# Performance work log

Measured on AMD Instinct MI355X. Metric: run time of the kernel, lower is better.

The kernel has to match this reference:

```python
import jax, jax.numpy as jnp
import numpy as np

EMBED_DIM = 1024
HEAD_DIM = 64


def setup_inputs() -> dict:
    key = jax.random.key(0)
    ks = jax.random.split(key, 7)
    B, S = 4, 2048
    s = 1.0 / np.sqrt(EMBED_DIM)
    h = jax.random.normal(ks[0], (B, S, EMBED_DIM), dtype=jnp.float32)
    Wq = jax.random.normal(ks[1], (EMBED_DIM, HEAD_DIM), dtype=jnp.float32) * s
    bq = jax.random.normal(ks[2], (HEAD_DIM,), dtype=jnp.float32) * 0.01
    Wk = jax.random.normal(ks[3], (EMBED_DIM, HEAD_DIM), dtype=jnp.float32) * s
    bk = jax.random.normal(ks[4], (HEAD_DIM,), dtype=jnp.float32) * 0.01
    Wv = jax.random.normal(ks[5], (EMBED_DIM, HEAD_DIM), dtype=jnp.float32) * s
    bv = jax.random.normal(ks[6], (HEAD_DIM,), dtype=jnp.float32) * 0.01
    return {"h": h, "Wq": Wq, "bq": bq, "Wk": Wk, "bk": bk, "Wv": Wv, "bv": bv}


def reference(h, Wq, bq, Wk, bk, Wv, bv):
    # Linear projections: h [B,S,E] -> q,k [B,S,D]
    q = jnp.einsum("bse,ed->bsd", h, Wq) + bq
    k = jnp.einsum("bse,ed->bsd", h, Wk) + bk
    v = jnp.einsum("bse,ed->bsd", h, Wv) + bv  # computed but UNUSED (faithful to source)
    del v
    scale = 1.0 / jnp.sqrt(jnp.asarray(HEAD_DIM, dtype=q.dtype))
    # scores [B, Sq, Sk]
    scores = jnp.einsum("bqd,bkd->bqk", q, k) * scale
    # NOTE: source uses softmax over dim=1 (query axis), not the key axis
    weights = jax.nn.softmax(scores, axis=1)
    # NOTE: source passes h (not v) as the value tensor
    out = jnp.einsum("bqk,bke->bqe", weights, h)  # [B, Sq, E]
    return out
```

## Files before the change

kernel.cpp:

```cpp
#include <hip/hip_runtime.h>
#include <hip/hip_bf16.h>
#include <math.h>

#define EMBED 1024
#define HDIM  64
#define BATCH 4
#define SEQ   2048

typedef __attribute__((ext_vector_type(8))) short short8;
typedef __attribute__((ext_vector_type(4))) float f32x4;
typedef unsigned int u32;
typedef unsigned short u16;

static __device__ __forceinline__ u16 f2bf(float f) {
    union { float f; u32 u; } v; v.f = f;
    u32 r = v.u + 0x7fffu + ((v.u >> 16) & 1u);
    return (u16)(r >> 16);
}

static __device__ __forceinline__ void gload_lds16(const u16* g, u16* l) {
    __builtin_amdgcn_global_load_lds(
        (const __attribute__((address_space(1))) u32*)g,
        (__attribute__((address_space(3))) u32*)l, 16, 0, 0);
}

__global__ __launch_bounds__(256) void wt_kernel(
    const float* __restrict__ Wq, const float* __restrict__ Wk,
    u16* __restrict__ WqT, u16* __restrict__ WkT, float* __restrict__ lsum)
{
    __shared__ float tile[64][65];
    const float* W = blockIdx.y ? Wk : Wq;
    u16* WT = blockIdx.y ? WkT : WqT;
    int e0 = blockIdx.x * 64;
    int t = threadIdx.x, c = t & 63, r4 = t >> 6;
    lsum[(blockIdx.y * 16 + blockIdx.x) * 256 + t] = 0.f;
    for (int r = r4; r < 64; r += 4)
        tile[r][c] = W[(size_t)(e0 + r) * HDIM + c];
    __syncthreads();
    for (int d = r4; d < 64; d += 4)
        WT[(size_t)d * EMBED + e0 + c] = f2bf(tile[c][d]);
}

__global__ __launch_bounds__(256) void proj_kernel(
    const float* __restrict__ h, const u16* __restrict__ WqT, const u16* __restrict__ WkT,
    const float* __restrict__ bq, const float* __restrict__ bk,
    u16* __restrict__ Qbf, u16* __restrict__ Kbf)
{
    __shared__ u16 hs[2][16][136];
    int b = blockIdx.x >> 7, s0 = (blockIdx.x & 127) * 16;
    int t = threadIdx.x, lane = t & 63, w = t >> 6;
    int l15 = lane & 15, quad = lane >> 4;
    int pj = w >> 1, nh = (w & 1) * 32;
    const float* hb = h + ((size_t)b * SEQ + s0) * EMBED;
    const u16* Wp = pj ? WkT : WqT;
    int r = t >> 4, c4 = (t & 15) * 4;

    f32x4 preA0 = *(const f32x4*)(hb + (size_t)r * EMBED + c4);
    f32x4 preA1 = *(const f32x4*)(hb + (size_t)r * EMBED + 64 + c4);
    f32x4 preB0 = *(const f32x4*)(hb + (size_t)r * EMBED + 128 + c4);
    f32x4 preB1 = *(const f32x4*)(hb + (size_t)r * EMBED + 192 + c4);
    f32x4 accA[2], accB[2];
    accA[0] = accA[1] = accB[0] = accB[1] = (f32x4){0.f, 0.f, 0.f, 0.f};

    const u16* Wrow0 = Wp + (size_t)(nh + l15) * EMBED;
    const u16* Wrow1 = Wp + (size_t)(nh + 16 + l15) * EMBED;

    short8 cw[8];
#pragma unroll
    for (int i = 0; i < 4; i++) {
        cw[i]     = *(const short8*)(Wrow0 + i * 32 + quad * 8);
        cw[4 + i] = *(const short8*)(Wrow1 + i * 32 + quad * 8);
    }

    for (int it = 0; it < 8; ++it) {
        int ec = it * 128, buf = it & 1;
        uint2 pk;
        pk.x = (u32)f2bf(preA0[0]) | ((u32)f2bf(preA0[1]) << 16);
        pk.y = (u32)f2bf(preA0[2]) | ((u32)f2bf(preA0[3]) << 16);
        *(uint2*)&hs[buf][r][c4] = pk;
        pk.x = (u32)f2bf(preA1[0]) | ((u32)f2bf(preA1[1]) << 16);
        pk.y = (u32)f2bf(preA1[2]) | ((u32)f2bf(preA1[3]) << 16);
        *(uint2*)&hs[buf][r][64 + c4] = pk;
        __syncthreads();

        preA0 = preB0; preA1 = preB1;
        if (it + 2 < 8) {
            preB0 = *(const f32x4*)(hb + (size_t)r * EMBED + ec + 256 + c4);
            preB1 = *(const f32x4*)(hb + (size_t)r * EMBED + ec + 320 + c4);
        }
        short8 nw[8];
#pragma unroll
        for (int i = 0; i < 8; i++) nw[i] = cw[i];
        if (it + 1 < 8) {
#pragma unroll
            for (int i = 0; i < 4; i++) {
                nw[i]     = *(const short8*)(Wrow0 + ec + 128 + i * 32 + quad * 8);
                nw[4 + i] = *(const short8*)(Wrow1 + ec + 128 + i * 32 + quad * 8);
            }
        }

        short8 a0 = *(const short8*)&hs[buf][l15][quad * 8];
        short8 a1 = *(const short8*)&hs[buf][l15][32 + quad * 8];
        short8 a2 = *(const short8*)&hs[buf][l15][64 + quad * 8];
        short8 a3 = *(const short8*)&hs[buf][l15][96 + quad * 8];
        accA[0] = __builtin_amdgcn_mfma_f32_16x16x32_bf16(a0, cw[0], accA[0], 0, 0, 0);
        accA[1] = __builtin_amdgcn_mfma_f32_16x16x32_bf16(a0, cw[4], accA[1], 0, 0, 0);
        accB[0] = __builtin_amdgcn_mfma_f32_16x16x32_bf16(a1, cw[1], accB[0], 0, 0, 0);
        accB[1] = __builtin_amdgcn_mfma_f32_16x16x32_bf16(a1, cw[5], accB[1], 0, 0, 0);
        accA[0] = __builtin_amdgcn_mfma_f32_16x16x32_bf16(a2, cw[2], accA[0], 0, 0, 0);
        accA[1] = __builtin_amdgcn_mfma_f32_16x16x32_bf16(a2, cw[6], accA[1], 0, 0, 0);
        accB[0] = __builtin_amdgcn_mfma_f32_16x16x32_bf16(a3, cw[3], accB[0], 0, 0, 0);
        accB[1] = __builtin_amdgcn_mfma_f32_16x16x32_bf16(a3, cw[7], accB[1], 0, 0, 0);
#pragma unroll
        for (int i = 0; i < 8; i++) cw[i] = nw[i];
    }

    const float* bias = pj ? bk : bq;
    float scale = pj ? 1.0f : 0.125f;
    u16* outp = pj ? Kbf : Qbf;
    float bv0 = bias[nh + l15], bv1 = bias[nh + 16 + l15];
#pragma unroll
    for (int rr = 0; rr < 4; rr++) {
        size_t row = (size_t)b * SEQ + s0 + quad * 4 + rr;
        outp[row * HDIM + nh + l15]      = f2bf((accA[0][rr] + accB[0][rr] + bv0) * scale);
        outp[row * HDIM + nh + 16 + l15] = f2bf((accA[1][rr] + accB[1][rr] + bv1) * scale);
    }
}

__global__ __launch_bounds__(512) void sw_kernel(
    const u16* __restrict__ Qbf, const u16* __restrict__ Kbf,
    u16* __restrict__ Wmat, float* __restrict__ lsum)
{
    int b = blockIdx.z;
    int k0 = blockIdx.x * 64;
    int t = threadIdx.x, lane = t & 63, w = t >> 6;
    int l15 = lane & 15, quad = lane >> 4;
    const u16* Qb = Qbf + (size_t)b * SEQ * HDIM;
    const u16* Kb = Kbf + (size_t)b * SEQ * HDIM;
    u16* Wb = Wmat + (size_t)b * SEQ * SEQ;

    short8 kfr[4][2];
#pragma unroll
    for (int g = 0; g < 4; g++)
#pragma unroll
        for (int hh = 0; hh < 2; hh++)
            kfr[g][hh] = *(const short8*)(
                Kb + (size_t)(k0 + g * 16 + l15) * HDIM + hh * 32 + quad * 8);

    f32x4 lacc[4];
#pragma unroll
    for (int g = 0; g < 4; g++) lacc[g] = (f32x4){0.f, 0.f, 0.f, 0.f};

    int qs = (blockIdx.y * 8 + w) * 64;

#pragma unroll
    for (int half = 0; half < 2; ++half) {
        int q0 = qs + half * 32;
        short8 cf[2][2];
#pragma unroll
        for (int a = 0; a < 2; a++)
#pragma unroll
            for (int hh = 0; hh < 2; hh++)
                cf[a][hh] = *(const short8*)(
                    Qb + (size_t)(q0 + a * 16 + l15) * HDIM + hh * 32 + quad * 8);

        f32x4 acc[2][4];
#pragma unroll
        for (int a = 0; a < 2; a++)
#pragma unroll
            for (int g = 0; g < 4; g++) acc[a][g] = (f32x4){0.f, 0.f, 0.f, 0.f};
#pragma unroll
        for (int a = 0; a < 2; a++)
#pragma unroll
            for (int g = 0; g < 4; g++) {
                acc[a][g] = __builtin_amdgcn_mfma_f32_16x16x32_bf16(
                    kfr[g][0], cf[a][0], acc[a][g], 0, 0, 0);
                acc[a][g] = __builtin_amdgcn_mfma_f32_16x16x32_bf16(
                    kfr[g][1], cf[a][1], acc[a][g], 0, 0, 0);
            }
#pragma unroll
        for (int a = 0; a < 2; a++) {
            u16* wrow = Wb + (size_t)(q0 + a * 16 + l15) * SEQ + k0;
#pragma unroll
            for (int g = 0; g < 4; g++) {
                float e0 = __expf(acc[a][g][0]), e1 = __expf(acc[a][g][1]);
                float e2 = __expf(acc[a][g][2]), e3 = __expf(acc[a][g][3]);
                lacc[g][0] += e0; lacc[g][1] += e1;
                lacc[g][2] += e2; lacc[g][3] += e3;
                uint2 pk;
                pk.x = (u32)f2bf(e0) | ((u32)f2bf(e1) << 16);
                pk.y = (u32)f2bf(e2) | ((u32)f2bf(e3) << 16);
                *(uint2*)(wrow + g * 16 + quad * 4) = pk;
            }
        }
    }
#pragma unroll
    for (int m = 1; m <= 8; m <<= 1)
#pragma unroll
        for (int g = 0; g < 4; g++) {
            lacc[g][0] += __shfl_xor(lacc[g][0], m, 64);
            lacc[g][1] += __shfl_xor(lacc[g][1], m, 64);
            lacc[g][2] += __shfl_xor(lacc[g][2], m, 64);
            lacc[g][3] += __shfl_xor(lacc[g][3], m, 64);
        }
    if (l15 == 0) {
        float* lp = lsum + b * SEQ + k0 + quad * 4;
#pragma unroll
        for (int g = 0; g < 4; g++) {
            atomicAdd(lp + g * 16 + 0, lacc[g][0]);
            atomicAdd(lp + g * 16 + 1, lacc[g][1]);
            atomicAdd(lp + g * 16 + 2, lacc[g][2]);
            atomicAdd(lp + g * 16 + 3, lacc[g][3]);
        }
    }
}

__global__ __launch_bounds__(256) void tscale_kernel(
    const float* __restrict__ h, const float* __restrict__ lsum,
    u16* __restrict__ hT)
{
    __shared__ float tile[64][65];
    int b  = blockIdx.z;
    int s0 = blockIdx.x * 64, e0 = blockIdx.y * 64;
    int t = threadIdx.x;
    int r16 = t >> 4, c4 = (t & 15) * 4;
    const float* hb = h + (size_t)b * SEQ * EMBED;
#pragma unroll
    for (int rr = r16; rr < 64; rr += 16) {
        f32x4 v = *(const f32x4*)(hb + (size_t)(s0 + rr) * EMBED + e0 + c4);
        *(f32x4*)&tile[rr][c4] = v;
    }
    __syncthreads();
    f32x4 ls = *(const f32x4*)(lsum + b * SEQ + s0 + c4);
    f32x4 il4;
    il4[0] = __builtin_amdgcn_rcpf(ls[0]);
    il4[1] = __builtin_amdgcn_rcpf(ls[1]);
    il4[2] = __builtin_amdgcn_rcpf(ls[2]);
    il4[3] = __builtin_amdgcn_rcpf(ls[3]);
    u16* hTb = hT + (size_t)b * EMBED * SEQ;
#pragma unroll
    for (int er = r16; er < 64; er += 16) {
        u16 p0 = f2bf(tile[c4 + 0][er] * il4[0]);
        u16 p1 = f2bf(tile[c4 + 1][er] * il4[1]);
        u16 p2 = f2bf(tile[c4 + 2][er] * il4[2]);
        u16 p3 = f2bf(tile[c4 + 3][er] * il4[3]);
        uint2 pk;
        pk.x = (u32)p0 | ((u32)p1 << 16);
        pk.y = (u32)p2 | ((u32)p3 << 16);
        *(uint2*)(hTb + (size_t)(e0 + er) * SEQ + s0 + c4) = pk;
    }
}

__global__ __launch_bounds__(512, 2) void out_gemm_kernel(
    const u16* __restrict__ Wmat, const u16* __restrict__ hT, float* __restrict__ out)
{
    __shared__ __align__(16) char smem[3 * 49152];
    int b = blockIdx.z;
    int q0 = blockIdx.x * 256, e0 = blockIdx.y * 128;
    int t = threadIdx.x, lane = t & 63, w = t >> 6;
    int l15 = lane & 15, quad = lane >> 4;
    const u16* Wb  = Wmat + (size_t)b * SEQ * SEQ;
    const u16* hTb = hT + (size_t)b * EMBED * SEQ;
    int kf = w >> 2;
    int wm = (w >> 1) & 1, wn = w & 1;
    int wq = wm * 128, we = wn * 64;

    f32x4 acc[8][4];
#pragma unroll
    for (int i = 0; i < 8; i++)
#pragma unroll
        for (int j = 0; j < 4; j++) acc[i][j] = (f32x4){0.f, 0.f, 0.f, 0.f};

    int st_rl = lane >> 3;
    int st_pc = lane & 7;

    const u16* gA[4];
    const u16* gB[2];
#pragma unroll
    for (int ld = 0; ld < 4; ld++) {
        int row = w * 32 + ld * 8 + st_rl;
        int cg  = st_pc ^ (row & 7);
        gA[ld] = Wb + (size_t)(q0 + row) * SEQ + cg * 8;
    }
#pragma unroll
    for (int ld = 0; ld < 2; ld++) {
        int row = w * 16 + ld * 8 + st_rl;
        int cg  = st_pc ^ (row & 7);
        gB[ld] = hTb + (size_t)(e0 + row) * SEQ + cg * 8;
    }
    int dA[4], dB[2];
#pragma unroll
    for (int ld = 0; ld < 4; ld++) dA[ld] = (w * 32 + ld * 8) * 128 + lane * 16;
#pragma unroll
    for (int ld = 0; ld < 2; ld++) dB[ld] = 32768 + (w * 16 + ld * 8) * 128 + lane * 16;
    int offA[8], offB[4];
#pragma unroll
    for (int ii = 0; ii < 8; ii++) {
        int ra  = wq + ii * 16 + l15;
        int pca = (kf * 4 + quad) ^ (ra & 7);
        offA[ii] = ra * 128 + pca * 16;
    }
#pragma unroll
    for (int j = 0; j < 4; j++) {
        int rb  = we + j * 16 + l15;
        int pcb = (kf * 4 + quad) ^ (rb & 7);
        offB[j] = 32768 + rb * 128 + pcb * 16;
    }

#define STAGE_H1(si)                                                           \
    {                                                                          \
        gload_lds16(gA[0], (u16*)(smem + (si) * 49152 + dA[0]));               \
        gload_lds16(gA[1], (u16*)(smem + (si) * 49152 + dA[1]));               \
        gload_lds16(gB[0], (u16*)(smem + (si) * 49152 + dB[0]));               \
    }
#define STAGE_H2(si)                                                           \
    {                                                                          \
        gload_lds16(gA[2], (u16*)(smem + (si) * 49152 + dA[2]));               \
        gload_lds16(gA[3], (u16*)(smem + (si) * 49152 + dA[3]));               \
        gload_lds16(gB[1], (u16*)(smem + (si) * 49152 + dB[1]));               \
    }
#define ADV()                                                                  \
    {                                                                          \
        gA[0] += 64; gA[1] += 64; gA[2] += 64; gA[3] += 64;                    \
        gB[0] += 64; gB[1] += 64;                                              \
    }

#define MFMA16(i0)                                                             \
    {                                                                          \
        _Pragma("unroll")                                                      \
        for (int ii = 0; ii < 4; ii++)                                         \
            _Pragma("unroll")                                                  \
            for (int j = 0; j < 4; j++)                                        \
                acc[(i0) + ii][j] = __builtin_amdgcn_mfma_f32_16x16x32_bf16(   \
                    af[ii], bfr[j], acc[(i0) + ii][j], 0, 0, 0);               \
    }

#define TILE(si, si2, DO_STAGE, VMC)                                           \
    {                                                                          \
        const char* Sb = smem + (si) * 49152;                                  \
        short8 af[4], bfr[4];                                                  \
                                                                  \
        _Pragma("unroll")                                                      \
        for (int ii = 0; ii < 4; ii++)                                         \
            af[ii] = *(const short8*)(Sb + offA[ii]);                          \
        _Pragma("unroll")                                                      \
        for (int j = 0; j < 4; j++)                                            \
            bfr[j] = *(const short8*)(Sb + offB[j]);                           \
        if (DO_STAGE) STAGE_H1(si2)                                            \
        __builtin_amdgcn_s_barrier();                                          \
        asm volatile("s_waitcnt lgkmcnt(0)" ::: "memory");                     \
        __builtin_amdgcn_sched_barrier(0);                                     \
        __builtin_amdgcn_s_setprio(1);                                         \
        MFMA16(0)                                                              \
        __builtin_amdgcn_s_setprio(0);                                         \
        __builtin_amdgcn_s_barrier();                                          \
                                                                  \
        _Pragma("unroll")                                                      \
        for (int ii = 0; ii < 4; ii++)                                         \
            af[ii] = *(const short8*)(Sb + offA[4 + ii]);                      \
        if (DO_STAGE) { STAGE_H2(si2) ADV() }                                  \
        __builtin_amdgcn_s_barrier();                                          \
        asm volatile("s_waitcnt lgkmcnt(0)" ::: "memory");                     \
        __builtin_amdgcn_sched_barrier(0);                                     \
        __builtin_amdgcn_s_setprio(1);                                         \
        MFMA16(4)                                                              \
        __builtin_amdgcn_s_setprio(0);                                         \
        if ((VMC) == 6) { asm volatile("s_waitcnt vmcnt(6)" ::: "memory"); }   \
        else if ((VMC) == 0) { asm volatile("s_waitcnt vmcnt(0)" ::: "memory"); } \
        __builtin_amdgcn_s_barrier();                                          \
    }

    STAGE_H1(0) STAGE_H2(0) ADV()
    STAGE_H1(1) STAGE_H2(1) ADV()
    asm volatile("s_waitcnt vmcnt(6)" ::: "memory");
    __builtin_amdgcn_s_barrier();

    for (int g = 0; g < 10; ++g) {
        TILE(0, 2, true, 6)
        TILE(1, 0, true, 6)
        TILE(2, 1, true, 6)
    }
    TILE(0, 2, false, 0)
    TILE(1, 0, false, -1)
#undef TILE
#undef STAGE_H1
#undef STAGE_H2
#undef ADV
#undef MFMA16

    float* red = (float*)smem;
    if (w >= 4) {
        float* reg = red + (size_t)(w & 3) * 8192;
#pragma unroll
        for (int i = 0; i < 8; i++)
#pragma unroll
            for (int j = 0; j < 4; j++)
                *(f32x4*)(reg + ((i * 4 + j) * 64 + lane) * 4) = acc[i][j];
    }
    __syncthreads();
    if (w < 4) {
        float* reg = red + (size_t)w * 8192;
        float* outb = out + (size_t)b * SEQ * EMBED;
#pragma unroll
        for (int i = 0; i < 8; i++)
#pragma unroll
            for (int j = 0; j < 4; j++) {
                f32x4 o = *(const f32x4*)(reg + ((i * 4 + j) * 64 + lane) * 4);
                o += acc[i][j];
#pragma unroll
                for (int r = 0; r < 4; r++)
                    outb[(size_t)(q0 + wq + i * 16 + quad * 4 + r) * EMBED
                         + e0 + we + j * 16 + l15] = o[r];
            }
    }
}

extern "C" void kernel_launch(void* const* d_in, const int* in_sizes, int n_in,
                              void* d_out, int out_size, void* d_ws, size_t ws_size,
                              hipStream_t stream) {
    (void)in_sizes; (void)n_in; (void)out_size; (void)ws_size;
    const float* h  = (const float*)d_in[0];
    const float* Wq = (const float*)d_in[1];
    const float* bq = (const float*)d_in[2];
    const float* Wk = (const float*)d_in[3];
    const float* bk = (const float*)d_in[4];
    float* out = (float*)d_out;

    char* ws = (char*)d_ws;
    u16*   Qbf  = (u16*)(ws);
    u16*   Kbf  = (u16*)(ws + (1ull << 20));
    u16*   hT   = (u16*)(ws + (2ull << 20));
    float* lsum = (float*)(ws + (18ull << 20));
    u16*   WqT  = (u16*)(ws + (18ull << 20) + (128ull << 10));
    u16*   WkT  = (u16*)(ws + (18ull << 20) + (256ull << 10));
    u16*   Wmat = (u16*)(ws + (19ull << 20));

    hipLaunchKernelGGL(wt_kernel, dim3(16, 2), dim3(256), 0, stream,
                       Wq, Wk, WqT, WkT, lsum);
    hipLaunchKernelGGL(proj_kernel, dim3(512), dim3(256), 0, stream,
                       h, WqT, WkT, bq, bk, Qbf, Kbf);
    hipLaunchKernelGGL(sw_kernel, dim3(32, 4, 4), dim3(512), 0, stream,
                       Qbf, Kbf, Wmat, lsum);
    hipLaunchKernelGGL(tscale_kernel, dim3(32, 16, 4), dim3(256), 0, stream,
                       h, lsum, hT);
    hipLaunchKernelGGL(out_gemm_kernel, dim3(8, 8, 4), dim3(512), 0, stream,
                       Wmat, hT, out);
}
```

Before: 171.8 us.

## Recompute exp(QK^T) inside output GEMM instead of materializing weight matrix

Stops writing the bf16 exp(scores) matrix (B*S*S) to global memory. The column-sum pass becomes an LSE-only kernel, and the output GEMM recomputes exp(QK^T) per K tile in shared memory from Q registers and staged K. This removes a 32MB write and the matching read, at the cost of computing QK^T and exp twice and adding a barrier inside every tile. The GEMM tile changes to 128x256 with no split-K reduction, and the LDS layout changes to match.

```diff
diff --git a/kernel.cpp b/kernel.cpp
--- a/kernel.cpp
+++ b/kernel.cpp
@@ -127,9 +127,9 @@
     }
 }
 
-__global__ __launch_bounds__(512) void sw_kernel(
+__global__ __launch_bounds__(512) void lse_kernel(
     const u16* __restrict__ Qbf, const u16* __restrict__ Kbf,
-    u16* __restrict__ Wmat, float* __restrict__ lsum)
+    float* __restrict__ lsum)
 {
     int b = blockIdx.z;
     int k0 = blockIdx.x * 64;
@@ -137,7 +137,6 @@
     int l15 = lane & 15, quad = lane >> 4;
     const u16* Qb = Qbf + (size_t)b * SEQ * HDIM;
     const u16* Kb = Kbf + (size_t)b * SEQ * HDIM;
-    u16* Wb = Wmat + (size_t)b * SEQ * SEQ;
 
     short8 kfr[4][2];
 #pragma unroll
@@ -179,20 +178,14 @@
                     kfr[g][1], cf[a][1], acc[a][g], 0, 0, 0);
             }
 #pragma unroll
-        for (int a = 0; a < 2; a++) {
-            u16* wrow = Wb + (size_t)(q0 + a * 16 + l15) * SEQ + k0;
+        for (int a = 0; a < 2; a++)
 #pragma unroll
             for (int g = 0; g < 4; g++) {
-                float e0 = __expf(acc[a][g][0]), e1 = __expf(acc[a][g][1]);
-                float e2 = __expf(acc[a][g][2]), e3 = __expf(acc[a][g][3]);
-                lacc[g][0] += e0; lacc[g][1] += e1;
-                lacc[g][2] += e2; lacc[g][3] += e3;
-                uint2 pk;
-                pk.x = (u32)f2bf(e0) | ((u32)f2bf(e1) << 16);
-                pk.y = (u32)f2bf(e2) | ((u32)f2bf(e3) << 16);
-                *(uint2*)(wrow + g * 16 + quad * 4) = pk;
+                lacc[g][0] += __expf(acc[a][g][0]);
+                lacc[g][1] += __expf(acc[a][g][1]);
+                lacc[g][2] += __expf(acc[a][g][2]);
+                lacc[g][3] += __expf(acc[a][g][3]);
             }
-        }
     }
 #pragma unroll
     for (int m = 1; m <= 8; m <<= 1)
@@ -251,168 +244,193 @@
     }
 }
 
-__global__ __launch_bounds__(512, 2) void out_gemm_kernel(
-    const u16* __restrict__ Wmat, const u16* __restrict__ hT, float* __restrict__ out)
+__global__ __launch_bounds__(512, 2) void fused_kernel(
+    const u16* __restrict__ Qbf, const u16* __restrict__ Kbf,
+    const u16* __restrict__ hT, float* __restrict__ out)
 {
-    __shared__ __align__(16) char smem[3 * 49152];
+    __shared__ __align__(16) char smem[3 * 40960 + 16384];
     int b = blockIdx.z;
-    int q0 = blockIdx.x * 256, e0 = blockIdx.y * 128;
+    int q0 = blockIdx.x * 128, e0 = blockIdx.y * 256;
     int t = threadIdx.x, lane = t & 63, w = t >> 6;
     int l15 = lane & 15, quad = lane >> 4;
-    const u16* Wb  = Wmat + (size_t)b * SEQ * SEQ;
+    const u16* Qb  = Qbf + (size_t)b * SEQ * HDIM;
+    const u16* Kb  = Kbf + (size_t)b * SEQ * HDIM;
     const u16* hTb = hT + (size_t)b * EMBED * SEQ;
-    int kf = w >> 2;
-    int wm = (w >> 1) & 1, wn = w & 1;
-    int wq = wm * 128, we = wn * 64;
-
-    f32x4 acc[8][4];
-#pragma unroll
-    for (int i = 0; i < 8; i++)
+    int kgrp = w & 3, qh = w >> 2;
+    int en = w & 3;
+
+    f32x4 acc[4][4];
+#pragma unroll
+    for (int i = 0; i < 4; i++)
 #pragma unroll
         for (int j = 0; j < 4; j++) acc[i][j] = (f32x4){0.f, 0.f, 0.f, 0.f};
 
-    int st_rl = lane >> 3;
-    int st_pc = lane & 7;
-
-    const u16* gA[4];
-    const u16* gB[2];
+    short8 qf[4][2];
+#pragma unroll
+    for (int a = 0; a < 4; a++)
+#pragma unroll
+        for (int dh = 0; dh < 2; dh++)
+            qf[a][dh] = *(const short8*)(
+                Qb + (size_t)(q0 + qh * 64 + a * 16 + l15) * HDIM + dh * 32 + quad * 8);
+
+    int offK[2];
+#pragma unroll
+    for (int dh = 0; dh < 2; dh++) {
+        int kr = kgrp * 16 + l15;
+        int c  = (dh * 4 + quad) ^ (kr & 7);
+        offK[dh] = 32768 + kr * 128 + c * 16;
+    }
+    int offPw[4];
+#pragma unroll
+    for (int a = 0; a < 4; a++) {
+        int row = qh * 64 + a * 16 + l15;
+        int c   = (kgrp * 2 + (quad >> 1)) ^ (row & 7);
+        offPw[a] = 122880 + row * 128 + c * 16 + (quad & 1) * 8;
+    }
+    int offPA[2][4];
+#pragma unroll
+    for (int ks = 0; ks < 2; ks++)
+#pragma unroll
+        for (int i = 0; i < 4; i++) {
+            int row = qh * 64 + i * 16 + l15;
+            int c   = (ks * 4 + quad) ^ (row & 7);
+            offPA[ks][i] = 122880 + row * 128 + c * 16;
+        }
+    int offBT[2][4];
+#pragma unroll
+    for (int ks = 0; ks < 2; ks++)
+#pragma unroll
+        for (int j = 0; j < 4; j++) {
+            int row = en * 64 + j * 16 + l15;
+            int c   = (ks * 4 + quad) ^ (row & 7);
+            offBT[ks][j] = row * 128 + c * 16;
+        }
+
+    const u16* gH[4]; const u16* gK1;
+    int dH[4], dK;
 #pragma unroll
     for (int ld = 0; ld < 4; ld++) {
-        int row = w * 32 + ld * 8 + st_rl;
-        int cg  = st_pc ^ (row & 7);
-        gA[ld] = Wb + (size_t)(q0 + row) * SEQ + cg * 8;
-    }
-#pragma unroll
-    for (int ld = 0; ld < 2; ld++) {
-        int row = w * 16 + ld * 8 + st_rl;
-        int cg  = st_pc ^ (row & 7);
-        gB[ld] = hTb + (size_t)(e0 + row) * SEQ + cg * 8;
-    }
-    int dA[4], dB[2];
-#pragma unroll
-    for (int ld = 0; ld < 4; ld++) dA[ld] = (w * 32 + ld * 8) * 128 + lane * 16;
-#pragma unroll
-    for (int ld = 0; ld < 2; ld++) dB[ld] = 32768 + (w * 16 + ld * 8) * 128 + lane * 16;
-    int offA[8], offB[4];
-#pragma unroll
-    for (int ii = 0; ii < 8; ii++) {
-        int ra  = wq + ii * 16 + l15;
-        int pca = (kf * 4 + quad) ^ (ra & 7);
-        offA[ii] = ra * 128 + pca * 16;
-    }
-#pragma unroll
-    for (int j = 0; j < 4; j++) {
-        int rb  = we + j * 16 + l15;
-        int pcb = (kf * 4 + quad) ^ (rb & 7);
-        offB[j] = 32768 + rb * 128 + pcb * 16;
-    }
-
-#define STAGE_H1(si)                                                           \
+        int rowb = w * 32 + ld * 8;
+        int row  = rowb + (lane >> 3);
+        int cg   = (lane & 7) ^ (row & 7);
+        gH[ld] = hTb + (size_t)(e0 + row) * SEQ + cg * 8;
+        dH[ld] = rowb * 128 + lane * 16;
+    }
+    {
+        int rowb = w * 8;
+        int row  = rowb + (lane >> 3);
+        int cg   = (lane & 7) ^ (row & 7);
+        gK1 = Kb + (size_t)row * HDIM + cg * 8;
+        dK  = 32768 + rowb * 128 + lane * 16;
+    }
+
+#define STAGE(si)                                                              \
     {                                                                          \
-        gload_lds16(gA[0], (u16*)(smem + (si) * 49152 + dA[0]));               \
-        gload_lds16(gA[1], (u16*)(smem + (si) * 49152 + dA[1]));               \
-        gload_lds16(gB[0], (u16*)(smem + (si) * 49152 + dB[0]));               \
-    }
-#define STAGE_H2(si)                                                           \
-    {                                                                          \
-        gload_lds16(gA[2], (u16*)(smem + (si) * 49152 + dA[2]));               \
-        gload_lds16(gA[3], (u16*)(smem + (si) * 49152 + dA[3]));               \
-        gload_lds16(gB[1], (u16*)(smem + (si) * 49152 + dB[1]));               \
+        gload_lds16(gH[0], (u16*)(smem + (si) * 40960 + dH[0]));               \
+        gload_lds16(gH[1], (u16*)(smem + (si) * 40960 + dH[1]));               \
+        gload_lds16(gH[2], (u16*)(smem + (si) * 40960 + dH[2]));               \
+        gload_lds16(gH[3], (u16*)(smem + (si) * 40960 + dH[3]));               \
+        gload_lds16(gK1,   (u16*)(smem + (si) * 40960 + dK));                  \
     }
 #define ADV()                                                                  \
     {                                                                          \
-        gA[0] += 64; gA[1] += 64; gA[2] += 64; gA[3] += 64;                    \
-        gB[0] += 64; gB[1] += 64;                                              \
-    }
-
-#define MFMA16(i0)                                                             \
-    {                                                                          \
-        _Pragma("unroll")                                                      \
-        for (int ii = 0; ii < 4; ii++)                                         \
-            _Pragma("unroll")                                                  \
-            for (int j = 0; j < 4; j++)                                        \
-                acc[(i0) + ii][j] = __builtin_amdgcn_mfma_f32_16x16x32_bf16(   \
-                    af[ii], bfr[j], acc[(i0) + ii][j], 0, 0, 0);               \
+        gH[0] += 64; gH[1] += 64; gH[2] += 64; gH[3] += 64;                    \
+        gK1 += 64 * HDIM;                                                      \
     }
 
 #define TILE(si, si2, DO_STAGE, VMC)                                           \
     {                                                                          \
-        const char* Sb = smem + (si) * 49152;                                  \
-        short8 af[4], bfr[4];                                                  \
-                                                                  \
-        _Pragma("unroll")                                                      \
-        for (int ii = 0; ii < 4; ii++)                                         \
-            af[ii] = *(const short8*)(Sb + offA[ii]);                          \
+        char* Sb = smem + (si) * 40960;                                        \
+                                                        \
+        short8 kfr0 = *(const short8*)(Sb + offK[0]);                          \
+        short8 kfr1 = *(const short8*)(Sb + offK[1]);                          \
+        f32x4 sA[4];                                                           \
+        _Pragma("unroll")                                                      \
+        for (int a = 0; a < 4; a++)                                            \
+            sA[a] = __builtin_amdgcn_mfma_f32_16x16x32_bf16(                   \
+                kfr0, qf[a][0], (f32x4){0.f, 0.f, 0.f, 0.f}, 0, 0, 0);         \
+        _Pragma("unroll")                                                      \
+        for (int a = 0; a < 4; a++)                                            \
+            sA[a] = __builtin_amdgcn_mfma_f32_16x16x32_bf16(                   \
+                kfr1, qf[a][1], sA[a], 0, 0, 0);                               \
+        _Pragma("unroll")                                                      \
+        for (int a = 0; a < 4; a++) {                                          \
+            float x0 = __expf(sA[a][0]), x1 = __expf(sA[a][1]);                \
+            float x2 = __expf(sA[a][2]), x3 = __expf(sA[a][3]);                \
+            uint2 pk;                                                          \
+            pk.x = (u32)f2bf(x0) | ((u32)f2bf(x1) << 16);                      \
+            pk.y = (u32)f2bf(x2) | ((u32)f2bf(x3) << 16);                      \
+            *(uint2*)(smem + offPw[a]) = pk;                                   \
+        }                                                                      \
+        if (DO_STAGE) { STAGE(si2) ADV() }                                     \
+        asm volatile("s_waitcnt lgkmcnt(0)" ::: "memory");                     \
+        __builtin_amdgcn_sched_barrier(0);                                     \
+        __builtin_amdgcn_s_barrier();                                          \
+                                                       \
+        short8 paf[4], pbf[4];                                                 \
+        _Pragma("unroll")                                                      \
+        for (int i = 0; i < 4; i++)                                            \
+            paf[i] = *(const short8*)(smem + offPA[0][i]);                     \
         _Pragma("unroll")                                                      \
         for (int j = 0; j < 4; j++)                                            \
-            bfr[j] = *(const short8*)(Sb + offB[j]);                           \
-        if (DO_STAGE) STAGE_H1(si2)                                            \
-        __builtin_amdgcn_s_barrier();                                          \
+            pbf[j] = *(const short8*)(Sb + offBT[0][j]);                       \
         asm volatile("s_waitcnt lgkmcnt(0)" ::: "memory");                     \
         __builtin_amdgcn_sched_barrier(0);                                     \
         __builtin_amdgcn_s_setprio(1);                                         \
-        MFMA16(0)                                                              \
+        _Pragma("unroll")                                                      \
+        for (int i = 0; i < 4; i++)                                            \
+            _Pragma("unroll")                                                  \
+            for (int j = 0; j < 4; j++)                                        \
+                acc[i][j] = __builtin_amdgcn_mfma_f32_16x16x32_bf16(           \
+                    paf[i], pbf[j], acc[i][j], 0, 0, 0);                       \
         __builtin_amdgcn_s_setprio(0);                                         \
-        __builtin_amdgcn_s_barrier();                                          \
-                                                                  \
-        _Pragma("unroll")                                                      \
-        for (int ii = 0; ii < 4; ii++)                                         \
-            af[ii] = *(const short8*)(Sb + offA[4 + ii]);                      \
-        if (DO_STAGE) { STAGE_H2(si2) ADV() }                                  \
-        __builtin_amdgcn_s_barrier();                                          \
+        _Pragma("unroll")                                                      \
+        for (int i = 0; i < 4; i++)                                            \
+            paf[i] = *(const short8*)(smem + offPA[1][i]);                     \
+        _Pragma("unroll")                                                      \
+        for (int j = 0; j < 4; j++)                                            \
+            pbf[j] = *(const short8*)(Sb + offBT[1][j]);                       \
         asm volatile("s_waitcnt lgkmcnt(0)" ::: "memory");                     \
         __builtin_amdgcn_sched_barrier(0);                                     \
         __builtin_amdgcn_s_setprio(1);                                         \
-        MFMA16(4)                                                              \
+        _Pragma("unroll")                                                      \
+        for (int i = 0; i < 4; i++)                                            \
+            _Pragma("unroll")                                                  \
+            for (int j = 0; j < 4; j++)                                        \
+                acc[i][j] = __builtin_amdgcn_mfma_f32_16x16x32_bf16(           \
+                    paf[i], pbf[j], acc[i][j], 0, 0, 0);                       \
         __builtin_amdgcn_s_setprio(0);                                         \
-        if ((VMC) == 6) { asm volatile("s_waitcnt vmcnt(6)" ::: "memory"); }   \
+        if ((VMC) == 5) { asm volatile("s_waitcnt vmcnt(5)" ::: "memory"); }   \
         else if ((VMC) == 0) { asm volatile("s_waitcnt vmcnt(0)" ::: "memory"); } \
         __builtin_amdgcn_s_barrier();                                          \
     }
 
-    STAGE_H1(0) STAGE_H2(0) ADV()
-    STAGE_H1(1) STAGE_H2(1) ADV()
-    asm volatile("s_waitcnt vmcnt(6)" ::: "memory");
+    asm volatile("s_waitcnt vmcnt(0)" ::: "memory");
+    STAGE(0) ADV()
+    STAGE(1) ADV()
+    asm volatile("s_waitcnt vmcnt(5)" ::: "memory");
     __builtin_amdgcn_s_barrier();
 
     for (int g = 0; g < 10; ++g) {
-        TILE(0, 2, true, 6)
-        TILE(1, 0, true, 6)
-        TILE(2, 1, true, 6)
+        TILE(0, 2, true, 5)
+        TILE(1, 0, true, 5)
+        TILE(2, 1, true, 5)
     }
     TILE(0, 2, false, 0)
     TILE(1, 0, false, -1)
 #undef TILE
-#undef STAGE_H1
-#undef STAGE_H2
+#undef STAGE
 #undef ADV
-#undef MFMA16
-
-    float* red = (float*)smem;
-    if (w >= 4) {
-        float* reg = red + (size_t)(w & 3) * 8192;
-#pragma unroll
-        for (int i = 0; i < 8; i++)
-#pragma unroll
-            for (int j = 0; j < 4; j++)
-                *(f32x4*)(reg + ((i * 4 + j) * 64 + lane) * 4) = acc[i][j];
-    }
-    __syncthreads();
-    if (w < 4) {
-        float* reg = red + (size_t)w * 8192;
-        float* outb = out + (size_t)b * SEQ * EMBED;
-#pragma unroll
-        for (int i = 0; i < 8; i++)
-#pragma unroll
-            for (int j = 0; j < 4; j++) {
-                f32x4 o = *(const f32x4*)(reg + ((i * 4 + j) * 64 + lane) * 4);
-                o += acc[i][j];
-#pragma unroll
-                for (int r = 0; r < 4; r++)
-                    outb[(size_t)(q0 + wq + i * 16 + quad * 4 + r) * EMBED
-                         + e0 + we + j * 16 + l15] = o[r];
-            }
-    }
+
+    float* outb = out + (size_t)b * SEQ * EMBED;
+#pragma unroll
+    for (int i = 0; i < 4; i++)
+#pragma unroll
+        for (int j = 0; j < 4; j++)
+#pragma unroll
+            for (int r = 0; r < 4; r++)
+                outb[(size_t)(q0 + qh * 64 + i * 16 + quad * 4 + r) * EMBED
+                     + e0 + en * 64 + j * 16 + l15] = acc[i][j][r];
 }
 
 extern "C" void kernel_launch(void* const* d_in, const int* in_sizes, int n_in,
@@ -431,18 +449,18 @@
     u16*   Kbf  = (u16*)(ws + (1ull << 20));
     u16*   hT   = (u16*)(ws + (2ull << 20));
     float* lsum = (float*)(ws + (18ull << 20));
-    u16*   WqT  = (u16*)(ws + (18ull << 20) + (128ull << 10));
-    u16*   WkT  = (u16*)(ws + (18ull << 20) + (256ull << 10));
-    u16*   Wmat = (u16*)(ws + (19ull << 20));
 
     hipLaunchKernelGGL(wt_kernel, dim3(16, 2), dim3(256), 0, stream,
-                       Wq, Wk, WqT, WkT, lsum);
+                       Wq, Wk, (u16*)(ws + (18ull << 20) + (128ull << 10)),
+                       (u16*)(ws + (18ull << 20) + (256ull << 10)), lsum);
     hipLaunchKernelGGL(proj_kernel, dim3(512), dim3(256), 0, stream,
-                       h, WqT, WkT, bq, bk, Qbf, Kbf);
-    hipLaunchKernelGGL(sw_kernel, dim3(32, 4, 4), dim3(512), 0, stream,
-                       Qbf, Kbf, Wmat, lsum);
+                       h, (const u16*)(ws + (18ull << 20) + (128ull << 10)),
+                       (const u16*)(ws + (18ull << 20) + (256ull << 10)),
+                       bq, bk, Qbf, Kbf);
+    hipLaunchKernelGGL(lse_kernel, dim3(32, 4, 4), dim3(512), 0, stream,
+                       Qbf, Kbf, lsum);
     hipLaunchKernelGGL(tscale_kernel, dim3(32, 16, 4), dim3(256), 0, stream,
                        h, lsum, hT);
-    hipLaunchKernelGGL(out_gemm_kernel, dim3(8, 8, 4), dim3(512), 0, stream,
-                       Wmat, hT, out);
-}
+    hipLaunchKernelGGL(fused_kernel, dim3(16, 4, 4), dim3(512), 0, stream,
+                       Qbf, Kbf, hT, out);
+}
```

New measurement: 183.5 us. +6.8%, slower.
